# Optimization experiments

Hardware: AMD Instinct MI355X
Metric: run time of the kernel (lower is better)

The kernel has to match this reference:

```python
import jax, jax.numpy as jnp
import numpy as np

DIM = 1024
HEADS = 16
HEAD_DIM = DIM // HEADS
FFN = 4096
EPS = 1e-6


def layernorm(x, a, b):
    # torch: mean, std (unbiased, ddof=1), divide by (std + eps)
    mean = jnp.mean(x, axis=-1, keepdims=True)
    std = jnp.std(x, axis=-1, keepdims=True, ddof=1)
    return a * (x - mean) / (std + EPS) + b


def setup_inputs() -> dict:
    key = jax.random.key(0)
    ks = jax.random.split(key, 8)
    B, S = 2, 2048
    x = jax.random.normal(ks[0], (B, S, DIM), dtype=jnp.float32)
    mask = jnp.zeros((1, 1, S, S), dtype=jnp.float32)
    sc = 0.02
    wq = jax.random.normal(ks[1], (DIM, DIM), jnp.float32) * sc
    wk = jax.random.normal(ks[2], (DIM, DIM), jnp.float32) * sc
    wv = jax.random.normal(ks[3], (DIM, DIM), jnp.float32) * sc
    wo = jax.random.normal(ks[4], (DIM, DIM), jnp.float32) * sc
    w1 = jax.random.normal(ks[5], (FFN, DIM), jnp.float32) * sc
    w2 = jax.random.normal(ks[6], (DIM, FFN), jnp.float32) * sc
    a1 = jnp.ones((DIM,), jnp.float32)
    b1 = jnp.zeros((DIM,), jnp.float32)
    a2 = jnp.ones((DIM,), jnp.float32)
    b2 = jnp.zeros((DIM,), jnp.float32)
    return {"x": x, "mask": mask, "wq": wq, "wk": wk, "wv": wv, "wo": wo,
            "w1": w1, "w2": w2, "a1": a1, "b1": b1, "a2": a2, "b2": b2}


def reference(x, mask, wq, wk, wv, wo, w1, w2, a1, b1, a2, b2):
    B, S, _ = x.shape
    # QKV projections (Linear weight is [out, in]; y = x @ W.T)
    q = (x @ wq.T).reshape(B, S, HEADS, HEAD_DIM).transpose(0, 2, 1, 3)
    k = (x @ wk.T).reshape(B, S, HEADS, HEAD_DIM).transpose(0, 2, 1, 3)
    v = (x @ wv.T).reshape(B, S, HEADS, HEAD_DIM).transpose(0, 2, 1, 3)
    scores = jnp.einsum('bhqd,bhkd->bhqk', q, k) / np.sqrt(HEAD_DIM).astype(np.float32)
    scores = scores + mask
    probs = jax.nn.softmax(scores.astype(jnp.float32), axis=-1).astype(q.dtype)
    attn = jnp.einsum('bhqk,bhkd->bhqd', probs, v)
    attn = attn.transpose(0, 2, 1, 3).reshape(B, S, DIM)
    attn_out = attn @ wo.T
    attn_x = layernorm(x + attn_out, a1, b1)
    # FFN with exact (erf) GELU, matching nn.GELU default
    h = jax.nn.gelu(attn_x @ w1.T, approximate=False)
    ffn_out = h @ w2.T
    return layernorm(attn_x + ffn_out, a2, b2)
```

## Files before the change

### kernel.cpp

```cpp
#include <hip/hip_runtime.h>
#include <math.h>

typedef __bf16 bf16x8 __attribute__((ext_vector_type(8)));
typedef float  f32x4  __attribute__((ext_vector_type(4)));
typedef unsigned short us4 __attribute__((ext_vector_type(4)));

__device__ __forceinline__ unsigned short f2bf(float f) {
    union { float f; unsigned int u; } v; v.f = f;
    return (unsigned short)((v.u + 0x7FFFu + ((v.u >> 16) & 1u)) >> 16);
}
__device__ __forceinline__ float bf2f(unsigned short u) {
    union { unsigned int i; float f; } c; c.i = (unsigned)u << 16;
    return c.f;
}
__device__ __forceinline__ unsigned cvt_pk_bf16(float lo, float hi) {
    unsigned r;
    asm("v_cvt_pk_bf16_f32 %0, %1, %2" : "=v"(r) : "v"(lo), "v"(hi));
    return r;
}
__device__ __forceinline__ float exp2_raw(float x) {
    float r;
    asm("v_exp_f32 %0, %1" : "=v"(r) : "v"(x));
    return r;
}
__device__ __forceinline__ void gload_lds16(const unsigned short* g, unsigned short* l) {
    __builtin_amdgcn_global_load_lds((__attribute__((address_space(1))) void*)(g),
                                     (__attribute__((address_space(3))) void*)(l), 16, 0, 0);
}
#define MFMA16(a, b, c) __builtin_amdgcn_mfma_f32_16x16x32_bf16((a), (b), (c), 0, 0, 0)

__global__ __launch_bounds__(256)
void cast_all(const float* __restrict__ x, const float* __restrict__ wq,
              const float* __restrict__ wk, const float* __restrict__ wv,
              const float* __restrict__ wo, const float* __restrict__ w1,
              const float* __restrict__ w2,
              unsigned short* __restrict__ xb, unsigned short* __restrict__ wqkv,
              unsigned short* __restrict__ wob, unsigned short* __restrict__ w1b,
              unsigned short* __restrict__ w2b) {
    const int b = blockIdx.x;
    const float* src; unsigned short* dst; int off;
    if      (b <  4096) { src = x;  dst = xb;             off = b;         }
    else if (b <  5120) { src = wq; dst = wqkv;           off = b - 4096;  }
    else if (b <  6144) { src = wk; dst = wqkv + 1048576; off = b - 5120;  }
    else if (b <  7168) { src = wv; dst = wqkv + 2097152; off = b - 6144;  }
    else if (b <  8192) { src = wo; dst = wob;            off = b - 7168;  }
    else if (b < 12288) { src = w1; dst = w1b;            off = b - 8192;  }
    else                { src = w2; dst = w2b;            off = b - 12288; }
    const int i = off * 1024 + threadIdx.x * 4;
    const float4 v = *reinterpret_cast<const float4*>(src + i);
    us4 o = { f2bf(v.x), f2bf(v.y), f2bf(v.z), f2bf(v.w) };
    *reinterpret_cast<us4*>(dst + i) = o;
}

template<int EPI>
__global__ __launch_bounds__(512, 1)
void gemm8(const unsigned short* __restrict__ A, const unsigned short* __restrict__ B,
           void* __restrict__ Cout, int M, int N, int Ks, int Kc, int NBY) {
    __shared__ __align__(16) unsigned short Al[2][256 * 64];
    __shared__ __align__(16) unsigned short Bl[2][256 * 64];
    const int tid = threadIdx.x;
    const int l   = tid & 63;
    const int w   = tid >> 6;
    const int q15 = l & 15;
    const int g   = l >> 4;
    const int wr  = w >> 2;
    const int wc  = w & 3;
    const int hb  = wc >> 1;
    const int wg  = blockIdx.x;
    const int swz = (wg & 7) * (gridDim.x >> 3) + (wg >> 3);
    const int bm  = (swz / NBY) * 256;
    const int bn  = (swz % NBY) * 256;
    const int kbase = blockIdx.y * Kc;
    const int NT  = Kc >> 6;

    const int srow = tid >> 3;
    const int lc   = (tid & 7) ^ (srow & 7);
    const unsigned short* aS = A + (size_t)(bm + srow) * Ks + kbase + lc * 8;
    const unsigned short* bS = B + (size_t)(bn + srow) * Ks + kbase + lc * 8;
    const int wuni = tid & ~63;

    auto stgA = [&](int buf, int h, int T) {
#pragma unroll
        for (int j = 0; j < 2; ++j)
            gload_lds16(aS + (size_t)(h * 128 + j * 64) * Ks + T * 64,
                        &Al[0][0] + buf * 16384 + h * 8192 + (j * 512 + wuni) * 8);
    };
    auto stgB = [&](int buf, int h, int T) {
#pragma unroll
        for (int j = 0; j < 2; ++j)
            gload_lds16(bS + (size_t)(h * 128 + j * 64) * Ks + T * 64,
                        &Bl[0][0] + buf * 16384 + h * 8192 + (j * 512 + wuni) * 8);
    };

    const int xk0 = g ^ (q15 & 7);
    const int xk1 = xk0 ^ 4;
    const int aRd = (wr * 128 + q15) * 64;
    const int bRd = (hb * 128 + (wc & 1) * 64 + q15) * 64;

    f32x4 acc[8][4] = {};
    bf16x8 aF[4][2], bF[4][2];

    stgA(0, 0, 0); stgA(0, 1, 0); stgB(0, 0, 0); stgB(0, 1, 0);
    stgA(1, 0, 1); stgA(1, 1, 1);
    asm volatile("s_waitcnt vmcnt(4)" ::: "memory");
    __builtin_amdgcn_sched_barrier(0);
    __builtin_amdgcn_s_barrier();

    for (int T = 0; T < NT; ++T) {
        const int cur = T & 1, nxt = cur ^ 1;
        const unsigned short* Ac = &Al[0][0] + cur * 16384 + aRd;
        const unsigned short* Bc = &Bl[0][0] + cur * 16384 + bRd;

#pragma unroll
        for (int mi = 0; mi < 4; ++mi) {
            aF[mi][0] = *reinterpret_cast<const bf16x8*>(Ac + mi * 1024 + xk0 * 8);
            aF[mi][1] = *reinterpret_cast<const bf16x8*>(Ac + mi * 1024 + xk1 * 8);
        }
#pragma unroll
        for (int ni = 0; ni < 2; ++ni) {
            bF[ni][0] = *reinterpret_cast<const bf16x8*>(Bc + ni * 1024 + xk0 * 8);
            bF[ni][1] = *reinterpret_cast<const bf16x8*>(Bc + ni * 1024 + xk1 * 8);
        }
        if (T + 1 < NT) stgB(nxt, 0, T + 1);
        asm volatile("s_waitcnt lgkmcnt(0)" ::: "memory");
        __builtin_amdgcn_sched_barrier(0);
        __builtin_amdgcn_s_setprio(1);
#pragma unroll
        for (int mi = 0; mi < 4; ++mi)
#pragma unroll
            for (int ni = 0; ni < 2; ++ni) {
                acc[mi][ni] = MFMA16(aF[mi][0], bF[ni][0], acc[mi][ni]);
                acc[mi][ni] = MFMA16(aF[mi][1], bF[ni][1], acc[mi][ni]);
            }
        __builtin_amdgcn_s_setprio(0);
        __builtin_amdgcn_s_barrier();

#pragma unroll
        for (int ni = 2; ni < 4; ++ni) {
            bF[ni][0] = *reinterpret_cast<const bf16x8*>(Bc + ni * 1024 + xk0 * 8);
            bF[ni][1] = *reinterpret_cast<const bf16x8*>(Bc + ni * 1024 + xk1 * 8);
        }
        if (T + 1 < NT) stgB(nxt, 1, T + 1);
        asm volatile("s_waitcnt lgkmcnt(0)" ::: "memory");
        __builtin_amdgcn_sched_barrier(0);
        __builtin_amdgcn_s_setprio(1);
#pragma unroll
        for (int mi = 0; mi < 4; ++mi)
#pragma unroll
            for (int ni = 2; ni < 4; ++ni) {
                acc[mi][ni] = MFMA16(aF[mi][0], bF[ni][0], acc[mi][ni]);
                acc[mi][ni] = MFMA16(aF[mi][1], bF[ni][1], acc[mi][ni]);
            }
        __builtin_amdgcn_s_setprio(0);
        __builtin_amdgcn_s_barrier();

#pragma unroll
        for (int mi = 0; mi < 4; ++mi) {
            aF[mi][0] = *reinterpret_cast<const bf16x8*>(Ac + (4 + mi) * 1024 + xk0 * 8);
            aF[mi][1] = *reinterpret_cast<const bf16x8*>(Ac + (4 + mi) * 1024 + xk1 * 8);
        }
        asm volatile("s_waitcnt lgkmcnt(0)" ::: "memory");
        __builtin_amdgcn_sched_barrier(0);
        __builtin_amdgcn_s_setprio(1);
#pragma unroll
        for (int mi = 0; mi < 4; ++mi)
#pragma unroll
            for (int ni = 0; ni < 2; ++ni) {
                acc[4 + mi][ni] = MFMA16(aF[mi][0], bF[ni][0], acc[4 + mi][ni]);
                acc[4 + mi][ni] = MFMA16(aF[mi][1], bF[ni][1], acc[4 + mi][ni]);
            }
        __builtin_amdgcn_s_setprio(0);
        __builtin_amdgcn_s_barrier();

        if (T + 2 < NT) { stgA(cur, 0, T + 2); stgA(cur, 1, T + 2); }
        __builtin_amdgcn_s_setprio(1);
#pragma unroll
        for (int mi = 0; mi < 4; ++mi)
#pragma unroll
            for (int ni = 2; ni < 4; ++ni) {
                acc[4 + mi][ni] = MFMA16(aF[mi][0], bF[ni][0], acc[4 + mi][ni]);
                acc[4 + mi][ni] = MFMA16(aF[mi][1], bF[ni][1], acc[4 + mi][ni]);
            }
        __builtin_amdgcn_s_setprio(0);
        if (T + 1 < NT) {
            if (T + 2 < NT) {
                asm volatile("s_waitcnt vmcnt(4)" ::: "memory");
            } else {
                asm volatile("s_waitcnt vmcnt(0)" ::: "memory");
            }
            __builtin_amdgcn_sched_barrier(0);
            __builtin_amdgcn_s_barrier();
        }
    }

#pragma unroll
    for (int mi = 0; mi < 8; ++mi) {
#pragma unroll
        for (int ni = 0; ni < 4; ++ni) {
#pragma unroll
            for (int rr = 0; rr < 4; ++rr) {
                const int m = bm + wr * 128 + mi * 16 + (g << 2) + rr;
                const int n = bn + wc * 64 + ni * 16 + q15;
                const float v = acc[mi][ni][rr];
                if (EPI == 1) {
                    unsigned short* C = (unsigned short*)Cout;
                    const int s  = m & 2047;
                    const int bh = ((m >> 11) << 4) | ((n & 1023) >> 6);
                    const int d  = n & 63;
                    if (n < 1024)
                        C[(size_t)(bh * 2048 + s) * 64 + d] = f2bf(v * 0.18033688011112042f);
                    else if (n < 2048)
                        C[(size_t)4194304 + (size_t)(bh * 2048 + s) * 64 + d] = f2bf(v);
                    else
                        C[(size_t)8388608 + ((size_t)bh * 64 + d) * 2048 + s] = f2bf(v);
                } else if (EPI == 2) {
                    const float gl = 0.5f * v * (1.0f + erff(v * 0.70710678118654752f));
                    ((unsigned short*)Cout)[(size_t)m * N + n] = f2bf(gl);
                } else {
                    ((unsigned short*)Cout)[(size_t)blockIdx.y * M * N + (size_t)m * N + n] = f2bf(v);
                }
            }
        }
    }
}

__global__ __launch_bounds__(512, 4)
void attn_kernel(const unsigned short* __restrict__ Q, const unsigned short* __restrict__ Kb,
                 const unsigned short* __restrict__ Vt, unsigned short* __restrict__ out) {
    __shared__ __align__(16) unsigned short kld[2][64 * 64];
    __shared__ __align__(16) unsigned short vld[2][64 * 64];
    __shared__ __align__(16) unsigned short plds[8][16][72];
    const int tid = threadIdx.x;
    const int l   = tid & 63;
    const int w   = tid >> 6;
    const int g   = l >> 4;
    const int q15 = l & 15;
    const int bh  = blockIdx.x & 31;
    const int qt  = blockIdx.x >> 5;
    const int q0  = qt * 128 + w * 16;
    const size_t base = (size_t)bh * 2048 * 64;

    bf16x8 qa0, qa1;
    {
        const unsigned short* qp = Q + base + (size_t)(q0 + q15) * 64 + g * 8;
        qa0 = *reinterpret_cast<const bf16x8*>(qp);
        qa1 = *reinterpret_cast<const bf16x8*>(qp + 32);
    }

    bf16x8 ones;
    {
        us4 o1 = { 0x3F80, 0x3F80, 0x3F80, 0x3F80 };
        bf16x8 t;
        *reinterpret_cast<us4*>(&t) = o1;
        *(reinterpret_cast<us4*>(&t) + 1) = o1;
        ones = t;
    }

    f32x4 oacc[5] = {};
    float mrun = -1e30f;

    auto stage = [&](int buf, int k0) {
        const int r  = tid >> 3;
        const int cs = (tid & 7) ^ (r & 7);
        gload_lds16(Kb + base + (size_t)(k0 + r) * 64 + cs * 8, &kld[buf][(tid & ~63) * 8]);
        gload_lds16(Vt + base + (size_t)r * 2048 + k0 + cs * 8, &vld[buf][(tid & ~63) * 8]);
    };

    stage(0, 0);
    int cur = 0;
    for (int t = 0; t < 32; ++t) {
        __syncthreads();
        if (t + 1 < 32) stage(cur ^ 1, (t + 1) * 64);

        bf16x8 kf[4][2];
#pragma unroll
        for (int ks = 0; ks < 4; ++ks) {
            const int row = ks * 16 + q15;
            const int sw  = row & 7;
            kf[ks][0] = *reinterpret_cast<const bf16x8*>(&kld[cur][row * 64 + ((g    ) ^ sw) * 8]);
            kf[ks][1] = *reinterpret_cast<const bf16x8*>(&kld[cur][row * 64 + ((4 + g) ^ sw) * 8]);
        }
        f32x4 sac[4];
#pragma unroll
        for (int ks = 0; ks < 4; ++ks) {
            f32x4 z = { 0.f, 0.f, 0.f, 0.f };
            z = MFMA16(kf[ks][0], qa0, z);
            z = MFMA16(kf[ks][1], qa1, z);
            sac[ks] = z;
        }

        float tm = fmaxf(fmaxf(sac[0][0], sac[0][1]), fmaxf(sac[0][2], sac[0][3]));
#pragma unroll
        for (int ks = 1; ks < 4; ++ks) {
            const float a = fmaxf(sac[ks][0], sac[ks][1]);
            const float b = fmaxf(sac[ks][2], sac[ks][3]);
            tm = fmaxf(tm, fmaxf(a, b));
        }
        tm = fmaxf(tm, __shfl_xor(tm, 16));
        tm = fmaxf(tm, __shfl_xor(tm, 32));
        const bool skip = __all(tm <= mrun + 8.0f);
        const float mnew = skip ? mrun : fmaxf(mrun, tm);
#pragma unroll
        for (int ks = 0; ks < 4; ++ks) {
            const float p0 = exp2_raw(sac[ks][0] - mnew);
            const float p1 = exp2_raw(sac[ks][1] - mnew);
            const float p2 = exp2_raw(sac[ks][2] - mnew);
            const float p3 = exp2_raw(sac[ks][3] - mnew);
            uint2 pk;
            pk.x = cvt_pk_bf16(p0, p1);
            pk.y = cvt_pk_bf16(p2, p3);
            *reinterpret_cast<uint2*>(&plds[w][q15][ks * 16 + g * 4]) = pk;
        }
        if (!skip) {
            const float sc = exp2_raw(mrun - mnew);
            float scr[4];
#pragma unroll
            for (int r = 0; r < 4; ++r) scr[r] = __shfl(sc, (l & 48) | (g * 4 + r));
#pragma unroll
            for (int j = 0; j < 5; ++j)
#pragma unroll
                for (int r = 0; r < 4; ++r) oacc[j][r] *= scr[r];
            mrun = mnew;
        }

        const bf16x8 pa0 = *reinterpret_cast<const bf16x8*>(&plds[w][q15][g * 8]);
        const bf16x8 pa1 = *reinterpret_cast<const bf16x8*>(&plds[w][q15][32 + g * 8]);
#pragma unroll
        for (int j = 0; j < 4; ++j) {
            const int row = j * 16 + q15;
            const int sw  = row & 7;
            const bf16x8 v0 = *reinterpret_cast<const bf16x8*>(&vld[cur][row * 64 + ((g    ) ^ sw) * 8]);
            const bf16x8 v1 = *reinterpret_cast<const bf16x8*>(&vld[cur][row * 64 + ((4 + g) ^ sw) * 8]);
            oacc[j] = MFMA16(pa0, v0, oacc[j]);
            oacc[j] = MFMA16(pa1, v1, oacc[j]);
        }
        oacc[4] = MFMA16(pa0, ones, oacc[4]);
        oacc[4] = MFMA16(pa1, ones, oacc[4]);
        cur ^= 1;
    }

    const int b = bh >> 4, h = bh & 15;
#pragma unroll
    for (int r = 0; r < 4; ++r) {
        const float inv = 1.f / oacc[4][r];
        const int q = q0 + g * 4 + r;
#pragma unroll
        for (int j = 0; j < 4; ++j)
            out[(size_t)(b * 2048 + q) * 1024 + h * 64 + j * 16 + q15] = f2bf(oacc[j][r] * inv);
    }
}

template<int NP>
__global__ __launch_bounds__(256)
void ln_res(const float* __restrict__ X, const unsigned short* __restrict__ P,
            const float* __restrict__ gamma, const float* __restrict__ beta,
            float* __restrict__ o32, unsigned short* __restrict__ o16) {
    __shared__ float red[4];
    const int t = threadIdx.x;
    const size_t row = blockIdx.x;
    const float4 a = *reinterpret_cast<const float4*>(X + row * 1024 + t * 4);
    float v0 = a.x, v1 = a.y, v2 = a.z, v3 = a.w;
#pragma unroll
    for (int p = 0; p < NP; ++p) {
        const us4 rr = *reinterpret_cast<const us4*>(P + (size_t)p * 4194304 + row * 1024 + t * 4);
        v0 += bf2f(rr.x); v1 += bf2f(rr.y); v2 += bf2f(rr.z); v3 += bf2f(rr.w);
    }
    float s = v0 + v1 + v2 + v3;
#pragma unroll
    for (int o = 1; o < 64; o <<= 1) s += __shfl_xor(s, o);
    if ((t & 63) == 0) red[t >> 6] = s;
    __syncthreads();
    const float mean = (red[0] + red[1] + red[2] + red[3]) * (1.f / 1024.f);
    v0 -= mean; v1 -= mean; v2 -= mean; v3 -= mean;
    float q = v0 * v0 + v1 * v1 + v2 * v2 + v3 * v3;
#pragma unroll
    for (int o = 1; o < 64; o <<= 1) q += __shfl_xor(q, o);
    __syncthreads();
    if ((t & 63) == 0) red[t >> 6] = q;
    __syncthreads();
    const float var = (red[0] + red[1] + red[2] + red[3]) * (1.f / 1023.f);
    const float inv = 1.f / (sqrtf(var) + 1e-6f);
    const float4 g  = *reinterpret_cast<const float4*>(gamma + t * 4);
    const float4 be = *reinterpret_cast<const float4*>(beta + t * 4);
    const float y0 = g.x * v0 * inv + be.x;
    const float y1 = g.y * v1 * inv + be.y;
    const float y2 = g.z * v2 * inv + be.z;
    const float y3 = g.w * v3 * inv + be.w;
    float4 o4; o4.x = y0; o4.y = y1; o4.z = y2; o4.w = y3;
    *reinterpret_cast<float4*>(o32 + row * 1024 + t * 4) = o4;
    if (o16) {
        us4 ob = { f2bf(y0), f2bf(y1), f2bf(y2), f2bf(y3) };
        *reinterpret_cast<us4*>(o16 + row * 1024 + t * 4) = ob;
    }
}

extern "C" void kernel_launch(void* const* d_in, const int* in_sizes, int n_in,
                              void* d_out, int out_size, void* d_ws, size_t ws_size,
                              hipStream_t stream) {
    const float* x  = (const float*)d_in[0];
    const float* wq = (const float*)d_in[2];
    const float* wk = (const float*)d_in[3];
    const float* wv = (const float*)d_in[4];
    const float* wo = (const float*)d_in[5];
    const float* w1 = (const float*)d_in[6];
    const float* w2 = (const float*)d_in[7];
    const float* a1 = (const float*)d_in[8];
    const float* b1 = (const float*)d_in[9];
    const float* a2 = (const float*)d_in[10];
    const float* b2 = (const float*)d_in[11];

    char* ws = (char*)d_ws;
    const size_t MB = 1024 * 1024;
    unsigned short* xb      = (unsigned short*)(ws);
    unsigned short* wqkv    = (unsigned short*)(ws + 8  * MB);
    unsigned short* wob     = (unsigned short*)(ws + 14 * MB);
    unsigned short* hbuf    = (unsigned short*)(ws);
    unsigned short* w1b     = (unsigned short*)(ws + 32 * MB);
    unsigned short* w2b     = (unsigned short*)(ws + 40 * MB);
    unsigned short* qkv     = (unsigned short*)(ws + 48 * MB);
    unsigned short* projp   = (unsigned short*)(ws + 48 * MB);
    unsigned short* ffn2p   = (unsigned short*)(ws + 48 * MB);
    unsigned short* attn    = (unsigned short*)(ws + 80 * MB);
    float*          attn_x  = (float*)(ws + 88 * MB);
    unsigned short* attn_xb = (unsigned short*)(ws + 104 * MB);

    cast_all<<<16384, 256, 0, stream>>>(x, wq, wk, wv, wo, w1, w2, xb, wqkv, wob, w1b, w2b);
    gemm8<1><<<dim3(192, 1), 512, 0, stream>>>(xb, wqkv, qkv, 4096, 3072, 1024, 1024, 12);
    attn_kernel<<<512, 512, 0, stream>>>(qkv, qkv + 4194304, qkv + 8388608, attn);
    gemm8<3><<<dim3(64, 4), 512, 0, stream>>>(attn, wob, projp, 4096, 1024, 1024, 256, 4);
    ln_res<4><<<4096, 256, 0, stream>>>(x, projp, a1, b1, attn_x, attn_xb);
    gemm8<2><<<dim3(256, 1), 512, 0, stream>>>(attn_xb, w1b, hbuf, 4096, 4096, 1024, 1024, 16);
    gemm8<3><<<dim3(64, 4), 512, 0, stream>>>(hbuf, w2b, ffn2p, 4096, 1024, 4096, 1024, 4);
    ln_res<4><<<4096, 256, 0, stream>>>(attn_x, ffn2p, a2, b2, (float*)d_out, nullptr);
}
```

Measured before the change: 254.6 us.

## Restructure GEMM prefetch into four interleaved half-tile stages per iteration

Replaces the previous scheme (prefetching A two tiles ahead and B one tile ahead) with a uniform one-tile-ahead prefetch. The next tile's four half-tiles (A0, B0, B1, A1) are each issued before one of the four MFMA phases, with a vmcnt(4) wait and barrier after each phase. On the last iteration it wraps around and redundantly loads tile 0 instead of branching, so the loop body has no conditionals. The intent is finer-grained overlap of global-to-LDS loads with MFMA work, at the cost of extra barriers and wasted loads on the final iteration.

```diff
diff --git a/kernel.cpp b/kernel.cpp
--- a/kernel.cpp
+++ b/kernel.cpp
@@ -28,6 +28,10 @@
                                      (__attribute__((address_space(3))) void*)(l), 16, 0, 0);
 }
 #define MFMA16(a, b, c) __builtin_amdgcn_mfma_f32_16x16x32_bf16((a), (b), (c), 0, 0, 0)
+#define LGKM0_FENCED()  do { asm volatile("s_waitcnt lgkmcnt(0)" ::: "memory"); \
+                             __builtin_amdgcn_sched_barrier(0); } while (0)
+#define VMC_FENCED(n)   do { asm volatile("s_waitcnt vmcnt(" #n ")" ::: "memory"); \
+                             __builtin_amdgcn_sched_barrier(0); } while (0)
 
 __global__ __launch_bounds__(256)
 void cast_all(const float* __restrict__ x, const float* __restrict__ wq,
@@ -100,14 +104,13 @@
     f32x4 acc[8][4] = {};
     bf16x8 aF[4][2], bF[4][2];
 
-    stgA(0, 0, 0); stgA(0, 1, 0); stgB(0, 0, 0); stgB(0, 1, 0);
-    stgA(1, 0, 1); stgA(1, 1, 1);
-    asm volatile("s_waitcnt vmcnt(4)" ::: "memory");
-    __builtin_amdgcn_sched_barrier(0);
+    stgA(0, 0, 0); stgB(0, 0, 0); stgB(0, 1, 0); stgA(0, 1, 0);
+    VMC_FENCED(4);
     __builtin_amdgcn_s_barrier();
 
     for (int T = 0; T < NT; ++T) {
         const int cur = T & 1, nxt = cur ^ 1;
+        const int Tn = (T + 1 < NT) ? T + 1 : 0;
         const unsigned short* Ac = &Al[0][0] + cur * 16384 + aRd;
         const unsigned short* Bc = &Bl[0][0] + cur * 16384 + bRd;
 
@@ -121,9 +124,9 @@
             bF[ni][0] = *reinterpret_cast<const bf16x8*>(Bc + ni * 1024 + xk0 * 8);
             bF[ni][1] = *reinterpret_cast<const bf16x8*>(Bc + ni * 1024 + xk1 * 8);
         }
-        if (T + 1 < NT) stgB(nxt, 0, T + 1);
-        asm volatile("s_waitcnt lgkmcnt(0)" ::: "memory");
-        __builtin_amdgcn_sched_barrier(0);
+        stgA(nxt, 0, Tn);
+        __builtin_amdgcn_s_barrier();
+        LGKM0_FENCED();
         __builtin_amdgcn_s_setprio(1);
 #pragma unroll
         for (int mi = 0; mi < 4; ++mi)
@@ -133,6 +136,7 @@
                 acc[mi][ni] = MFMA16(aF[mi][1], bF[ni][1], acc[mi][ni]);
             }
         __builtin_amdgcn_s_setprio(0);
+        VMC_FENCED(4);
         __builtin_amdgcn_s_barrier();
 
 #pragma unroll
@@ -140,9 +144,9 @@
             bF[ni][0] = *reinterpret_cast<const bf16x8*>(Bc + ni * 1024 + xk0 * 8);
             bF[ni][1] = *reinterpret_cast<const bf16x8*>(Bc + ni * 1024 + xk1 * 8);
         }
-        if (T + 1 < NT) stgB(nxt, 1, T + 1);
-        asm volatile("s_waitcnt lgkmcnt(0)" ::: "memory");
-        __builtin_amdgcn_sched_barrier(0);
+        stgB(nxt, 0, Tn);
+        __builtin_amdgcn_s_barrier();
+        LGKM0_FENCED();
         __builtin_amdgcn_s_setprio(1);
 #pragma unroll
         for (int mi = 0; mi < 4; ++mi)
@@ -152,6 +156,7 @@
                 acc[mi][ni] = MFMA16(aF[mi][1], bF[ni][1], acc[mi][ni]);
             }
         __builtin_amdgcn_s_setprio(0);
+        VMC_FENCED(4);
         __builtin_amdgcn_s_barrier();
 
 #pragma unroll
@@ -159,8 +164,9 @@
             aF[mi][0] = *reinterpret_cast<const bf16x8*>(Ac + (4 + mi) * 1024 + xk0 * 8);
             aF[mi][1] = *reinterpret_cast<const bf16x8*>(Ac + (4 + mi) * 1024 + xk1 * 8);
         }
-        asm volatile("s_waitcnt lgkmcnt(0)" ::: "memory");
-        __builtin_amdgcn_sched_barrier(0);
+        stgB(nxt, 1, Tn);
+        __builtin_amdgcn_s_barrier();
+        LGKM0_FENCED();
         __builtin_amdgcn_s_setprio(1);
 #pragma unroll
         for (int mi = 0; mi < 4; ++mi)
@@ -172,7 +178,8 @@
         __builtin_amdgcn_s_setprio(0);
         __builtin_amdgcn_s_barrier();
 
-        if (T + 2 < NT) { stgA(cur, 0, T + 2); stgA(cur, 1, T + 2); }
+        stgA(nxt, 1, Tn);
+        __builtin_amdgcn_s_barrier();
         __builtin_amdgcn_s_setprio(1);
 #pragma unroll
         for (int mi = 0; mi < 4; ++mi)
@@ -182,16 +189,10 @@
                 acc[4 + mi][ni] = MFMA16(aF[mi][1], bF[ni][1], acc[4 + mi][ni]);
             }
         __builtin_amdgcn_s_setprio(0);
-        if (T + 1 < NT) {
-            if (T + 2 < NT) {
-                asm volatile("s_waitcnt vmcnt(4)" ::: "memory");
-            } else {
-                asm volatile("s_waitcnt vmcnt(0)" ::: "memory");
-            }
-            __builtin_amdgcn_sched_barrier(0);
-            __builtin_amdgcn_s_barrier();
-        }
-    }
+        VMC_FENCED(4);
+        __builtin_amdgcn_s_barrier();
+    }
+    asm volatile("s_waitcnt vmcnt(0)" ::: "memory");
 
 #pragma unroll
     for (int mi = 0; mi < 8; ++mi) {
```

New measurement: 262.7 us. 1.03x slower.
